# Optimization experiments

Measured on AMD Instinct MI355X. Metric: run time of the kernel, lower is better.

## Reference

```python
import jax, jax.numpy as jnp
import numpy as np
import math

NUM_HEADS = 16
ROPE_BASE = 10000.0
SLIDING_WINDOW = 512  # note: original triu-then-tril composition makes the mask empty (no-op)


def _rope_cos_sin(seq_len, head_dim, dtype):
    inv_freq = 1.0 / (ROPE_BASE ** (jnp.arange(0, head_dim, 2, dtype=jnp.float32) / head_dim))
    t = jnp.arange(seq_len, dtype=jnp.float32)
    freqs = t[:, None] * inv_freq[None, :]          # [S, D/2]
    emb = jnp.concatenate([freqs, freqs], axis=-1)  # [S, D]
    # reshape to broadcast over [B, S, H, D]
    return jnp.cos(emb)[None, :, None, :].astype(dtype), jnp.sin(emb)[None, :, None, :].astype(dtype)


def _rotate_half(x):
    x1, x2 = jnp.split(x, 2, axis=-1)
    return jnp.concatenate([-x2, x1], axis=-1)


def setup_inputs() -> dict:
    key = jax.random.key(0)
    ks = jax.random.split(key, 9)
    B, S, E = 2, 2048, 2048
    sc = 1.0 / math.sqrt(E)
    return {
        "hidden_states": jax.random.normal(ks[0], (B, S, E), dtype=jnp.float32),
        "Wq": jax.random.normal(ks[1], (E, E), dtype=jnp.float32) * sc,
        "bq": jax.random.normal(ks[2], (E,), dtype=jnp.float32) * 0.01,
        "Wk": jax.random.normal(ks[3], (E, E), dtype=jnp.float32) * sc,
        "bk": jax.random.normal(ks[4], (E,), dtype=jnp.float32) * 0.01,
        "Wv": jax.random.normal(ks[5], (E, E), dtype=jnp.float32) * sc,
        "bv": jax.random.normal(ks[6], (E,), dtype=jnp.float32) * 0.01,
        "Wo": jax.random.normal(ks[7], (E, E), dtype=jnp.float32) * sc,
        "bo": jax.random.normal(ks[8], (E,), dtype=jnp.float32) * 0.01,
    }


def reference(hidden_states, Wq, bq, Wk, bk, Wv, bv, Wo, bo):
    B, S, E = hidden_states.shape
    H = NUM_HEADS
    D = E // H
    q = (hidden_states @ Wq.T + bq).reshape(B, S, H, D)
    k = (hidden_states @ Wk.T + bk).reshape(B, S, H, D)
    v = (hidden_states @ Wv.T + bv).reshape(B, S, H, D)

    cos, sin = _rope_cos_sin(S, D, q.dtype)
    q = q * cos + _rotate_half(q) * sin
    k = k * cos + _rotate_half(k) * sin

    scale = 1.0 / math.sqrt(D)
    scores = jnp.einsum("bqhd,bkhd->bhqk", q, k) * scale  # [B,H,S,S]
    # Faithful to source: triu(ones, +w) followed by tril(..., -w) is empty -> mask is a no-op.
    attn = jax.nn.softmax(scores, axis=-1)
    out = jnp.einsum("bhqk,bkhd->bqhd", attn, v).reshape(B, S, E)
    return out @ Wo.T + bo
```

## Files before the change

kernel.cpp:

```cpp
#include <hip/hip_runtime.h>
#include <hip/hip_bf16.h>

#define B_ 2
#define S_ 2048
#define E_ 2048
#define H_ 16
#define D_ 128
#define M_ (B_*S_)
#define NQKV_ (3*E_)

typedef __attribute__((ext_vector_type(8))) short bf16x8;
typedef __attribute__((ext_vector_type(4))) float f32x4;
typedef __attribute__((ext_vector_type(4))) unsigned short u16x4;
typedef __attribute__((ext_vector_type(2))) unsigned u32x2;

__device__ __forceinline__ unsigned short f2bf(float f) {
  union { float f; unsigned u; } v; v.f = f;
  unsigned r = v.u + 0x7fffu + ((v.u >> 16) & 1u);
  return (unsigned short)(r >> 16);
}
__device__ __forceinline__ float bf2f(unsigned short h) {
  union { unsigned u; float f; } v; v.u = ((unsigned)h) << 16;
  return v.f;
}

__device__ __forceinline__ void gload_lds16(const void* g, void* l) {
  __builtin_amdgcn_global_load_lds(
      (const __attribute__((address_space(1))) unsigned*)g,
      (__attribute__((address_space(3))) unsigned*)l, 16, 0, 0);
}

__global__ __launch_bounds__(256) void prep_kernel(
    const float* __restrict__ hs,
    const float* __restrict__ Wq, const float* __restrict__ Wk, const float* __restrict__ Wv,
    const float* __restrict__ Wo,
    const float* __restrict__ bq, const float* __restrict__ bk, const float* __restrict__ bv,
    unsigned short* __restrict__ hsb, unsigned short* __restrict__ Wqkv,
    unsigned short* __restrict__ Wob, float* __restrict__ biasqkv,
    float* __restrict__ cosT, float* __restrict__ sinT)
{
  const int seg = blockIdx.y;
  const int t0 = blockIdx.x * 256 + threadIdx.x;
  const int stride = gridDim.x * 256;
  if (seg == 0) {
    const int n = (M_*E_)/4;
    for (int i = t0; i < n; i += stride) {
      f32x4 v = ((const f32x4*)hs)[i];
      u16x4 o; o[0]=f2bf(v[0]); o[1]=f2bf(v[1]); o[2]=f2bf(v[2]); o[3]=f2bf(v[3]);
      ((u16x4*)hsb)[i] = o;
    }
  } else if (seg == 1) {
    const int n = (3*E_*E_)/4;
    for (int i = t0; i < n; i += stride) {
      int e4 = i << 2;
      int r = e4 >> 11;
      int k = e4 & 2047;
      const float* src = (r < E_) ? (Wq + ((size_t)r << 11) + k)
                       : (r < 2*E_) ? (Wk + ((size_t)(r - E_) << 11) + k)
                       : (Wv + ((size_t)(r - 2*E_) << 11) + k);
      f32x4 v = *(const f32x4*)src;
      u16x4 o; o[0]=f2bf(v[0]); o[1]=f2bf(v[1]); o[2]=f2bf(v[2]); o[3]=f2bf(v[3]);
      ((u16x4*)Wqkv)[i] = o;
    }
  } else if (seg == 2) {
    const int n = (E_*E_)/4;
    for (int i = t0; i < n; i += stride) {
      f32x4 v = ((const f32x4*)Wo)[i];
      u16x4 o; o[0]=f2bf(v[0]); o[1]=f2bf(v[1]); o[2]=f2bf(v[2]); o[3]=f2bf(v[3]);
      ((u16x4*)Wob)[i] = o;
    }
  } else if (seg == 3) {
    for (int i = t0; i < NQKV_; i += stride)
      biasqkv[i] = (i < E_) ? bq[i] : (i < 2*E_) ? bk[i - E_] : bv[i - 2*E_];
  } else {
    for (int i = t0; i < S_*64; i += stride) {
      int j = i & 63, s = i >> 6;
      float inv = exp2f(-(float)j * (13.287712379549449f / 64.0f));
      float ang = (float)s * inv;
      cosT[i] = cosf(ang);
      sinT[i] = sinf(ang);
    }
  }
}

#define STAGE8(basePtr, BUF, AB, KS, KT) do { \
    unsigned short* dst_ = lds + (BUF)*32768 + (AB)*16384 + (KS)*8192; \
    const unsigned short* src_ = (basePtr) + (KT)*64 + (KS)*32; \
    _Pragma("unroll") \
    for (int j_ = 0; j_ < 2; ++j_) { \
      int cc_ = (j_ << 9) + tid; \
      int row_ = cc_ >> 2, c2_ = cc_ & 3; \
      int sc_ = c2_ ^ ((row_ >> 1) & 3); \
      gload_lds16(src_ + (size_t)row_*K + sc_*8, (char*)dst_ + cc_*16); \
    } } while(0)

#define LDA8(DST, MH, KS, BUF) do { \
    const unsigned short* Ab_ = lds + (BUF)*32768 + (KS)*8192; \
    _Pragma("unroll") \
    for (int j_ = 0; j_ < 4; ++j_) { \
      int row_ = wr*128 + ((MH)*4 + j_)*16 + l15; \
      DST[j_] = *(const bf16x8*)(Ab_ + row_*32 + ((l4 ^ ((row_>>1)&3)) << 3)); \
    } } while(0)

#define LDB8(DST, KS, BUF) do { \
    const unsigned short* Bb_ = lds + (BUF)*32768 + 16384 + (KS)*8192; \
    _Pragma("unroll") \
    for (int j_ = 0; j_ < 4; ++j_) { \
      int row_ = wc*64 + j_*16 + l15; \
      DST[j_] = *(const bf16x8*)(Bb_ + row_*32 + ((l4 ^ ((row_>>1)&3)) << 3)); \
    } } while(0)

#define EPSW(col, row) ((col) ^ ((((row) >> 2) & 3) << 3))

__global__ __launch_bounds__(512, 2) void gemm8(
    const unsigned short* __restrict__ A,
    const unsigned short* __restrict__ Bm,
    const float* __restrict__ bias,
    unsigned short* __restrict__ Cv,
    const float* __restrict__ cosT, const float* __restrict__ sinT,
    int M, int N, int K, int ldc, int nq)
{
  __shared__ __align__(16) unsigned short lds[65536];
  const int tid = threadIdx.x;
  const int lane = tid & 63;
  const int w = tid >> 6;
  const int wr = w >> 2, wc = w & 3;
  const int l15 = lane & 15, l4 = lane >> 4;

  const int ntile = N >> 8;
  int wg = blockIdx.x;
  const int cpx = gridDim.x >> 3;
  wg = (wg & 7) * cpx + (wg >> 3);
  const int tm = wg / ntile, tn = wg % ntile;

  const unsigned short* Abase = A + ((size_t)tm*256)*K;
  const unsigned short* Bbase = Bm + ((size_t)tn*256)*K;

  f32x4 acc[8][4] = {};

  const int NT = K >> 6;

  STAGE8(Bbase, 0, 1, 0, 0); STAGE8(Abase, 0, 0, 0, 0);
  STAGE8(Bbase, 0, 1, 1, 0); STAGE8(Abase, 0, 0, 1, 0);
  __builtin_amdgcn_sched_barrier(0);
  asm volatile("s_waitcnt vmcnt(0)" ::: "memory");
  __builtin_amdgcn_s_barrier();

  for (int t = 0; t < NT; ++t) {
    const int cb = t & 1;
    const bool more = (t + 1 < NT);
    if (more) {
      STAGE8(Bbase, cb^1, 1, 0, t+1); STAGE8(Abase, cb^1, 0, 0, t+1);
      STAGE8(Bbase, cb^1, 1, 1, t+1); STAGE8(Abase, cb^1, 0, 1, t+1);
    }
    __builtin_amdgcn_sched_barrier(0);
    #pragma unroll
    for (int ks = 0; ks < 2; ++ks) {
      bf16x8 a0[4], a1[4], bv[4];
      LDA8(a0, 0, ks, cb);
      LDA8(a1, 1, ks, cb);
      LDB8(bv, ks, cb);
      #pragma unroll
      for (int mm = 0; mm < 4; ++mm)
        #pragma unroll
        for (int nn = 0; nn < 4; ++nn)
          acc[mm][nn] = __builtin_amdgcn_mfma_f32_16x16x32_bf16(a0[mm], bv[nn], acc[mm][nn], 0,0,0);
      #pragma unroll
      for (int mm = 0; mm < 4; ++mm)
        #pragma unroll
        for (int nn = 0; nn < 4; ++nn)
          acc[4+mm][nn] = __builtin_amdgcn_mfma_f32_16x16x32_bf16(a1[mm], bv[nn], acc[4+mm][nn], 0,0,0);
    }
    if (more) {
      asm volatile("s_waitcnt vmcnt(0)" ::: "memory");
      __builtin_amdgcn_s_barrier();
    }
  }

  const bool isQ = (tn*256) < nq;
  const float QSC = 0.08838834764831845f * 1.4426950408889634f;

  __syncthreads();

  #pragma unroll
  for (int mt = 0; mt < 8; ++mt) {
    #pragma unroll
    for (int nt = 0; nt < 4; ++nt) {
      int col = wc*64 + nt*16 + l15;
      float bvv = bias[tn*256 + col];
      #pragma unroll
      for (int r = 0; r < 4; ++r) {
        int row = wr*128 + mt*16 + l4*4 + r;
        lds[row*256 + EPSW(col, row)] = f2bf(acc[mt][nt][r] + bvv);
      }
    }
  }
  __syncthreads();

  #pragma unroll
  for (int mt = 0; mt < 8; ++mt) {
    #pragma unroll
    for (int nt = 0; nt < 4; ++nt) {
      int col = wc*64 + nt*16 + l15;
      int colg = tn*256 + col;
      int j = col & 63;
      bool hi = (col >> 6) & 1;
      float bvv = bias[colg];
      #pragma unroll
      for (int r = 0; r < 4; ++r) {
        int row = wr*128 + mt*16 + l4*4 + r;
        int rowg = tm*256 + row;
        int s = rowg & (S_-1);
        float x = bf2f(f2bf(acc[mt][nt][r] + bvv));
        float pp = bf2f(lds[row*256 + EPSW(col ^ 64, row)]);
        float c = cosT[s*64 + j], sn = sinT[s*64 + j];
        float o = hi ? (x*c + pp*sn) : (x*c - pp*sn);
        if (isQ) o *= QSC;
        Cv[(size_t)rowg*ldc + colg] = f2bf(o);
      }
    }
  }
}

#define STGA(BUFP, TKT, KS) do { \
    unsigned short* dst_ = lds + (BUFP)*24576 + (KS)*4096; \
    const unsigned short* src_ = Abase + (TKT)*64 + (KS)*32; \
    int cc_ = tid; int row_ = cc_ >> 2, c2_ = cc_ & 3; \
    int sc_ = c2_ ^ ((row_ >> 1) & 3); \
    gload_lds16(src_ + (size_t)row_*K + sc_*8, (char*)dst_ + cc_*16); \
  } while(0)

#define STGB(BUFP, TKT, KS) do { \
    unsigned short* dst_ = lds + (BUFP)*24576 + 8192 + (KS)*8192; \
    const unsigned short* src_ = Bbase + (TKT)*64 + (KS)*32; \
    _Pragma("unroll") \
    for (int j_ = 0; j_ < 2; ++j_) { \
      int cc_ = (j_ << 9) + tid; int row_ = cc_ >> 2, c2_ = cc_ & 3; \
      int sc_ = c2_ ^ ((row_ >> 1) & 3); \
      gload_lds16(src_ + (size_t)row_*K + sc_*8, (char*)dst_ + cc_*16); \
    } } while(0)

template<int OUT_F32>
__global__ __launch_bounds__(512, 2) void gemmA(
    const unsigned short* __restrict__ A,
    const unsigned short* __restrict__ Bm,
    const float* __restrict__ bias,
    void* __restrict__ Cv,
    int M, int N, int K, int ldc)
{
  __shared__ __align__(16) unsigned short lds[73728];
  const int tid = threadIdx.x;
  const int lane = tid & 63;
  const int w = tid >> 6;
  const int wr = w >> 2, wc = w & 3;
  const int l15 = lane & 15, l4 = lane >> 4;

  const int ntile = N >> 8;
  int wg = blockIdx.x;
  const int cpx = gridDim.x >> 3;
  wg = (wg & 7) * cpx + (wg >> 3);
  const int tm = wg / ntile, tn = wg % ntile;

  const unsigned short* Abase = A + ((size_t)tm*128)*K;
  const unsigned short* Bbase = Bm + ((size_t)tn*256)*K;

  f32x4 acc[4][4] = {};

  const int NT = K >> 6;

  STGA(0,0,0); STGB(0,0,0); STGA(0,0,1); STGB(0,0,1);
  STGA(1,1,0); STGB(1,1,0); STGA(1,1,1); STGB(1,1,1);
  __builtin_amdgcn_sched_barrier(0);
  asm volatile("s_waitcnt vmcnt(6)" ::: "memory");
  __builtin_amdgcn_s_barrier();

  int bufc = 0, bufn = 2;
  for (int i = 0; i < NT; ++i) {
    const bool st = (i + 2 < NT);
    const bool more = (i + 1 < NT);
    if (st) { STGA(bufn, i+2, 0); STGB(bufn, i+2, 0); STGA(bufn, i+2, 1); STGB(bufn, i+2, 1); }
    __builtin_amdgcn_sched_barrier(0);
    #pragma unroll
    for (int ks = 0; ks < 2; ++ks) {
      bf16x8 af[4], bv[4];
      { const unsigned short* Ab_ = lds + bufc*24576 + ks*4096;
        #pragma unroll
        for (int j = 0; j < 4; ++j) {
          int row = wr*64 + j*16 + l15;
          af[j] = *(const bf16x8*)(Ab_ + row*32 + ((l4 ^ ((row>>1)&3)) << 3)); }
        const unsigned short* Bb_ = lds + bufc*24576 + 8192 + ks*8192;
        #pragma unroll
        for (int j = 0; j < 4; ++j) {
          int row = wc*64 + j*16 + l15;
          bv[j] = *(const bf16x8*)(Bb_ + row*32 + ((l4 ^ ((row>>1)&3)) << 3)); } }
      #pragma unroll
      for (int mm = 0; mm < 4; ++mm)
        #pragma unroll
        for (int nn = 0; nn < 4; ++nn)
          acc[mm][nn] = __builtin_amdgcn_mfma_f32_16x16x32_bf16(af[mm], bv[nn], acc[mm][nn], 0,0,0);
    }
    if (st)       { asm volatile("s_waitcnt vmcnt(6)" ::: "memory"); }
    else if (more){ asm volatile("s_waitcnt vmcnt(0)" ::: "memory"); }
    if (more) __builtin_amdgcn_s_barrier();
    bufc = (bufc + 1 == 3) ? 0 : bufc + 1;
    bufn = (bufn + 1 == 3) ? 0 : bufn + 1;
  }

  #pragma unroll
  for (int mt = 0; mt < 4; ++mt) {
    #pragma unroll
    for (int nt = 0; nt < 4; ++nt) {
      int colg = tn*256 + wc*64 + nt*16 + l15;
      float bvv = bias[colg];
      #pragma unroll
      for (int r = 0; r < 4; ++r) {
        int rowg = tm*128 + wr*64 + mt*16 + l4*4 + r;
        float v = acc[mt][nt][r] + bvv;
        if (OUT_F32) ((float*)Cv)[(size_t)rowg*ldc + colg] = v;
        else ((unsigned short*)Cv)[(size_t)rowg*ldc + colg] = f2bf(v);
      }
    }
  }
}

__global__ __launch_bounds__(256) void transv_kernel(
    const unsigned short* __restrict__ qkv, unsigned short* __restrict__ Vt)
{
  __shared__ unsigned short t[32][33];
  int bid = blockIdx.x;
  int st = bid & 63;
  int dt = (bid >> 6) & 3;
  int bh = bid >> 8;
  int b = bh >> 4, h = bh & 15;
  int tx = threadIdx.x & 31, ty = threadIdx.x >> 5;
  #pragma unroll
  for (int j = 0; j < 4; ++j) {
    int r = ty + j*8;
    t[r][tx] = qkv[(size_t)(b*S_ + st*32 + r)*NQKV_ + 2*E_ + h*128 + dt*32 + tx];
  }
  __syncthreads();
  #pragma unroll
  for (int j = 0; j < 4; ++j) {
    int r = ty + j*8;
    Vt[((size_t)bh*D_ + dt*32 + r)*S_ + st*32 + tx] = t[tx][r];
  }
}

__global__ __launch_bounds__(256, 2) void attn_kernel(
    const unsigned short* __restrict__ qkv, const unsigned short* __restrict__ Vt,
    unsigned short* __restrict__ Ao)
{
  __shared__ unsigned short lK[2][64*128];
  __shared__ unsigned short lV[2][128*64];
  __shared__ __align__(16) unsigned short lP[4*32*64];
  int bid = blockIdx.x;
  bid = (bid & 7)*64 + (bid >> 3);
  const int qt = bid & 15;
  const int bh = bid >> 4;
  const int b = bh >> 4, h = bh & 15;
  const int tid = threadIdx.x, lane = tid & 63, w = tid >> 6;
  const int l15 = lane & 15, l4 = lane >> 4;

  bf16x8 qf[2][4];
  #pragma unroll
  for (int g = 0; g < 2; ++g) {
    const int qrow = qt*128 + w*32 + g*16 + l15;
    const unsigned short* qp = qkv + (size_t)(b*S_ + qrow)*NQKV_ + h*128 + l4*8;
    #pragma unroll
    for (int f = 0; f < 4; ++f) qf[g][f] = *(const bf16x8*)(qp + f*32);
  }

  f32x4 O[2][8];
  #pragma unroll
  for (int g = 0; g < 2; ++g)
    #pragma unroll
    for (int i = 0; i < 8; ++i) O[g][i] = (f32x4){0.f,0.f,0.f,0.f};
  float mx[2] = {-1e30f,-1e30f}, lsum[2] = {0.f,0.f};

  unsigned short* myP = lP + w*(32*64);
  const int ksw = (l15 & 7) << 3;
  const size_t kbase = (size_t)b*S_*NQKV_ + E_ + (size_t)h*128;
  const size_t vbase = (size_t)bh*D_*S_;

  #define ASTAGE(bi, ktile) do { \
    _Pragma("unroll") \
    for (int i_ = 0; i_ < 4; ++i_) { \
      int cc_ = i_*256 + tid; \
      int row_ = cc_ >> 4, col_ = cc_ & 15; \
      int scol_ = col_ ^ (row_ & 7); \
      gload_lds16(qkv + kbase + (size_t)((ktile)*64 + row_)*NQKV_ + scol_*8, \
                  (char*)(&lK[bi][0]) + cc_*16); \
    } \
    _Pragma("unroll") \
    for (int i_ = 0; i_ < 4; ++i_) { \
      int cc_ = i_*256 + tid; \
      int row_ = cc_ >> 3, col_ = cc_ & 7; \
      int scol_ = col_ ^ ((row_ & 7) ^ ((row_ >> 3) & 7)); \
      gload_lds16(Vt + vbase + (size_t)row_*S_ + (ktile)*64 + scol_*8, \
                  (char*)(&lV[bi][0]) + cc_*16); \
    } } while(0)

  ASTAGE(0, 0);
  asm volatile("s_waitcnt vmcnt(0)" ::: "memory");
  __syncthreads();

  for (int it = 0; it < S_/64; ++it) {
    const int cur = it & 1;
    if (it + 1 < S_/64) ASTAGE(cur ^ 1, it + 1);
    __builtin_amdgcn_sched_barrier(0);

    f32x4 sfr[2][4];
    __builtin_amdgcn_s_setprio(1);
    #pragma unroll
    for (int nf = 0; nf < 4; ++nf) {
      f32x4 s0 = (f32x4){0.f,0.f,0.f,0.f};
      f32x4 s1 = (f32x4){0.f,0.f,0.f,0.f};
      #pragma unroll
      for (int ks = 0; ks < 4; ++ks) {
        int row = nf*16 + l15;
        int ch = (ks*4 + l4) ^ (row & 7);
        bf16x8 kf = *(const bf16x8*)(&lK[cur][0] + row*128 + ch*8);
        s0 = __builtin_amdgcn_mfma_f32_16x16x32_bf16(kf, qf[0][ks], s0, 0, 0, 0);
        s1 = __builtin_amdgcn_mfma_f32_16x16x32_bf16(kf, qf[1][ks], s1, 0, 0, 0);
      }
      sfr[0][nf] = s0; sfr[1][nf] = s1;
    }
    __builtin_amdgcn_s_setprio(0);

    float vm[2];
    #pragma unroll
    for (int g = 0; g < 2; ++g) {
      float v = -1e30f;
      #pragma unroll
      for (int nf = 0; nf < 4; ++nf)
        #pragma unroll
        for (int r = 0; r < 4; ++r) v = fmaxf(v, sfr[g][nf][r]);
      v = fmaxf(v, __shfl_xor(v, 16, 64));
      v = fmaxf(v, __shfl_xor(v, 32, 64));
      vm[g] = v;
    }

    if (__any((vm[0] > mx[0] + 8.0f) || (vm[1] > mx[1] + 8.0f))) {
      #pragma unroll
      for (int g = 0; g < 2; ++g) {
        float mn = fmaxf(mx[g], vm[g]);
        float al = __builtin_amdgcn_exp2f(mx[g] - mn);
        mx[g] = mn;
        lsum[g] *= al;
        #pragma unroll
        for (int r = 0; r < 4; ++r) {
          float ar = __shfl(al, (lane & 48) + l4*4 + r, 64);
          #pragma unroll
          for (int df = 0; df < 8; ++df) O[g][df][r] *= ar;
        }
      }
    }

    #pragma unroll
    for (int g = 0; g < 2; ++g) {
      float ps = 0.f;
      #pragma unroll
      for (int nf = 0; nf < 4; ++nf) {
        #pragma unroll
        for (int r = 0; r < 4; ++r) {
          float p = __builtin_amdgcn_exp2f(sfr[g][nf][r] - mx[g]);
          sfr[g][nf][r] = p;
          ps += p;
        }
      }
      ps += __shfl_xor(ps, 16, 64);
      ps += __shfl_xor(ps, 32, 64);
      lsum[g] += ps;
    }

    #pragma unroll
    for (int g = 0; g < 2; ++g) {
      #pragma unroll
      for (int nf = 0; nf < 4; ++nf) {
        unsigned lo, hi;
        asm("v_cvt_pk_bf16_f32 %0, %1, %2" : "=v"(lo) : "v"(sfr[g][nf][0]), "v"(sfr[g][nf][1]));
        asm("v_cvt_pk_bf16_f32 %0, %1, %2" : "=v"(hi) : "v"(sfr[g][nf][2]), "v"(sfr[g][nf][3]));
        int k0 = (nf*16 + l4*4) ^ ksw;
        u32x2 val; val[0] = lo; val[1] = hi;
        *(u32x2*)(myP + (g*16 + l15)*64 + k0) = val;
      }
    }
    asm volatile("s_waitcnt lgkmcnt(0)" ::: "memory");

    __builtin_amdgcn_s_setprio(1);
    #pragma unroll
    for (int ks2 = 0; ks2 < 2; ++ks2) {
      int kk = (ks2*32 + l4*8) ^ ksw;
      bf16x8 pf0 = *(const bf16x8*)(myP + l15*64 + kk);
      bf16x8 pf1 = *(const bf16x8*)(myP + (16 + l15)*64 + kk);
      #pragma unroll
      for (int df = 0; df < 8; ++df) {
        int row = df*16 + l15;
        int ch = (ks2*4 + l4) ^ ((row & 7) ^ ((row >> 3) & 7));
        bf16x8 vf = *(const bf16x8*)(&lV[cur][0] + row*64 + ch*8);
        O[0][df] = __builtin_amdgcn_mfma_f32_16x16x32_bf16(pf0, vf, O[0][df], 0, 0, 0);
        O[1][df] = __builtin_amdgcn_mfma_f32_16x16x32_bf16(pf1, vf, O[1][df], 0, 0, 0);
      }
    }
    __builtin_amdgcn_s_setprio(0);
    asm volatile("s_waitcnt vmcnt(0)" ::: "memory");
    __syncthreads();
  }

  #pragma unroll
  for (int g = 0; g < 2; ++g) {
    float linv = 1.0f / lsum[g];
    float inv[4];
    #pragma unroll
    for (int r = 0; r < 4; ++r) inv[r] = __shfl(linv, (lane & 48) + l4*4 + r, 64);
    #pragma unroll
    for (int df = 0; df < 8; ++df) {
      int colg = h*128 + df*16 + l15;
      #pragma unroll
      for (int r = 0; r < 4; ++r) {
        int rowg = qt*128 + w*32 + g*16 + l4*4 + r;
        Ao[(size_t)(b*S_ + rowg)*E_ + colg] = f2bf(O[g][df][r] * inv[r]);
      }
    }
  }
}

extern "C" void kernel_launch(void* const* d_in, const int* in_sizes, int n_in,
                              void* d_out, int out_size, void* d_ws, size_t ws_size,
                              hipStream_t stream) {
  const float* hs = (const float*)d_in[0];
  const float* Wq = (const float*)d_in[1];
  const float* bq = (const float*)d_in[2];
  const float* Wk = (const float*)d_in[3];
  const float* bk = (const float*)d_in[4];
  const float* Wv = (const float*)d_in[5];
  const float* bv = (const float*)d_in[6];
  const float* Wo = (const float*)d_in[7];
  const float* bo = (const float*)d_in[8];
  float* out = (float*)d_out;

  char* p = (char*)d_ws;
  auto alloc = [&](size_t bytes) { char* r = p; p += (bytes + 255) & ~(size_t)255; return r; };
  unsigned short* hsb  = (unsigned short*)alloc((size_t)M_*E_*2);
  unsigned short* Wqkv = (unsigned short*)alloc((size_t)NQKV_*E_*2);
  unsigned short* Wob  = (unsigned short*)alloc((size_t)E_*E_*2);
  unsigned short* qkv  = (unsigned short*)alloc((size_t)M_*NQKV_*2);
  unsigned short* Vt   = (unsigned short*)alloc((size_t)B_*H_*D_*S_*2);
  unsigned short* Ao   = (unsigned short*)alloc((size_t)M_*E_*2);
  float* biasqkv = (float*)alloc((size_t)NQKV_*4);
  float* cosT = (float*)alloc((size_t)S_*64*4);
  float* sinT = (float*)alloc((size_t)S_*64*4);

  prep_kernel<<<dim3(2048, 5), 256, 0, stream>>>(hs, Wq, Wk, Wv, Wo, bq, bk, bv,
      hsb, Wqkv, Wob, biasqkv, cosT, sinT);
  gemm8<<<dim3((M_/256)*(2*E_/256)), 512, 0, stream>>>(
      hsb, Wqkv, biasqkv, qkv, cosT, sinT, M_, 2*E_, E_, NQKV_, E_);
  gemmA<0><<<dim3((M_/128)*(E_/256)), 512, 0, stream>>>(
      hsb, Wqkv + (size_t)2*E_*E_, biasqkv + 2*E_, qkv + 2*E_, M_, E_, E_, NQKV_);
  transv_kernel<<<dim3(B_*H_*(D_/32)*(S_/32)), 256, 0, stream>>>(qkv, Vt);
  attn_kernel<<<dim3(B_*H_*(S_/128)), 256, 0, stream>>>(qkv, Vt, Ao);
  gemmA<1><<<dim3((M_/128)*(E_/256)), 512, 0, stream>>>(
      Ao, Wob, bo, out, M_, E_, E_, E_);
}
```

Baseline: 272.1 us.

## Fuse V transpose into V projection GEMM epilogue via LDS

Replaces the separate V GEMM plus transpose kernel with a single GEMM whose epilogue stages the bf16 tile in swizzled LDS and writes V directly in the transposed [B,H,D,S] layout. This removes one kernel launch and a full read and write of V through global memory. The K loop is moved into a shared macro so both GEMMs reuse it. The epilogue adds an extra LDS round trip and barrier, and the qkv V slice is no longer written.

After: 264.9 us. 1.03x faster.

```diff
diff --git a/kernel.cpp b/kernel.cpp
--- a/kernel.cpp
+++ b/kernel.cpp
@@ -240,6 +240,44 @@
       gload_lds16(src_ + (size_t)row_*K + sc_*8, (char*)dst_ + cc_*16); \
     } } while(0)
 
+#define GEMMA_KLOOP() do { \
+  STGA(0,0,0); STGB(0,0,0); STGA(0,0,1); STGB(0,0,1); \
+  STGA(1,1,0); STGB(1,1,0); STGA(1,1,1); STGB(1,1,1); \
+  __builtin_amdgcn_sched_barrier(0); \
+  asm volatile("s_waitcnt vmcnt(6)" ::: "memory"); \
+  __builtin_amdgcn_s_barrier(); \
+  int bufc = 0, bufn = 2; \
+  for (int i = 0; i < NT; ++i) { \
+    const bool st = (i + 2 < NT); \
+    const bool more = (i + 1 < NT); \
+    if (st) { STGA(bufn, i+2, 0); STGB(bufn, i+2, 0); STGA(bufn, i+2, 1); STGB(bufn, i+2, 1); } \
+    __builtin_amdgcn_sched_barrier(0); \
+    _Pragma("unroll") \
+    for (int ks = 0; ks < 2; ++ks) { \
+      bf16x8 af[4], bvv[4]; \
+      { const unsigned short* Ab_ = lds + bufc*24576 + ks*4096; \
+        _Pragma("unroll") \
+        for (int j = 0; j < 4; ++j) { \
+          int row = wr*64 + j*16 + l15; \
+          af[j] = *(const bf16x8*)(Ab_ + row*32 + ((l4 ^ ((row>>1)&3)) << 3)); } \
+        const unsigned short* Bb_ = lds + bufc*24576 + 8192 + ks*8192; \
+        _Pragma("unroll") \
+        for (int j = 0; j < 4; ++j) { \
+          int row = wc*64 + j*16 + l15; \
+          bvv[j] = *(const bf16x8*)(Bb_ + row*32 + ((l4 ^ ((row>>1)&3)) << 3)); } } \
+      _Pragma("unroll") \
+      for (int mm = 0; mm < 4; ++mm) \
+        _Pragma("unroll") \
+        for (int nn = 0; nn < 4; ++nn) \
+          acc[mm][nn] = __builtin_amdgcn_mfma_f32_16x16x32_bf16(af[mm], bvv[nn], acc[mm][nn], 0,0,0); \
+    } \
+    if (st)       { asm volatile("s_waitcnt vmcnt(6)" ::: "memory"); } \
+    else if (more){ asm volatile("s_waitcnt vmcnt(0)" ::: "memory"); } \
+    if (more) __builtin_amdgcn_s_barrier(); \
+    bufc = (bufc + 1 == 3) ? 0 : bufc + 1; \
+    bufn = (bufn + 1 == 3) ? 0 : bufn + 1; \
+  } } while(0)
+
 template<int OUT_F32>
 __global__ __launch_bounds__(512, 2) void gemmA(
     const unsigned short* __restrict__ A,
@@ -265,46 +303,9 @@
   const unsigned short* Bbase = Bm + ((size_t)tn*256)*K;
 
   f32x4 acc[4][4] = {};
-
   const int NT = K >> 6;
 
-  STGA(0,0,0); STGB(0,0,0); STGA(0,0,1); STGB(0,0,1);
-  STGA(1,1,0); STGB(1,1,0); STGA(1,1,1); STGB(1,1,1);
-  __builtin_amdgcn_sched_barrier(0);
-  asm volatile("s_waitcnt vmcnt(6)" ::: "memory");
-  __builtin_amdgcn_s_barrier();
-
-  int bufc = 0, bufn = 2;
-  for (int i = 0; i < NT; ++i) {
-    const bool st = (i + 2 < NT);
-    const bool more = (i + 1 < NT);
-    if (st) { STGA(bufn, i+2, 0); STGB(bufn, i+2, 0); STGA(bufn, i+2, 1); STGB(bufn, i+2, 1); }
-    __builtin_amdgcn_sched_barrier(0);
-    #pragma unroll
-    for (int ks = 0; ks < 2; ++ks) {
-      bf16x8 af[4], bv[4];
-      { const unsigned short* Ab_ = lds + bufc*24576 + ks*4096;
-        #pragma unroll
-        for (int j = 0; j < 4; ++j) {
-          int row = wr*64 + j*16 + l15;
-          af[j] = *(const bf16x8*)(Ab_ + row*32 + ((l4 ^ ((row>>1)&3)) << 3)); }
-        const unsigned short* Bb_ = lds + bufc*24576 + 8192 + ks*8192;
-        #pragma unroll
-        for (int j = 0; j < 4; ++j) {
-          int row = wc*64 + j*16 + l15;
-          bv[j] = *(const bf16x8*)(Bb_ + row*32 + ((l4 ^ ((row>>1)&3)) << 3)); } }
-      #pragma unroll
-      for (int mm = 0; mm < 4; ++mm)
-        #pragma unroll
-        for (int nn = 0; nn < 4; ++nn)
-          acc[mm][nn] = __builtin_amdgcn_mfma_f32_16x16x32_bf16(af[mm], bv[nn], acc[mm][nn], 0,0,0);
-    }
-    if (st)       { asm volatile("s_waitcnt vmcnt(6)" ::: "memory"); }
-    else if (more){ asm volatile("s_waitcnt vmcnt(0)" ::: "memory"); }
-    if (more) __builtin_amdgcn_s_barrier();
-    bufc = (bufc + 1 == 3) ? 0 : bufc + 1;
-    bufn = (bufn + 1 == 3) ? 0 : bufn + 1;
-  }
+  GEMMA_KLOOP();
 
   #pragma unroll
   for (int mt = 0; mt < 4; ++mt) {
@@ -323,26 +324,64 @@
   }
 }
 
-__global__ __launch_bounds__(256) void transv_kernel(
-    const unsigned short* __restrict__ qkv, unsigned short* __restrict__ Vt)
+__global__ __launch_bounds__(512, 2) void gemmVt(
+    const unsigned short* __restrict__ A,
+    const unsigned short* __restrict__ Bm,
+    const float* __restrict__ bias,
+    unsigned short* __restrict__ Vt,
+    int M, int N, int K)
 {
-  __shared__ unsigned short t[32][33];
-  int bid = blockIdx.x;
-  int st = bid & 63;
-  int dt = (bid >> 6) & 3;
-  int bh = bid >> 8;
-  int b = bh >> 4, h = bh & 15;
-  int tx = threadIdx.x & 31, ty = threadIdx.x >> 5;
-  #pragma unroll
-  for (int j = 0; j < 4; ++j) {
-    int r = ty + j*8;
-    t[r][tx] = qkv[(size_t)(b*S_ + st*32 + r)*NQKV_ + 2*E_ + h*128 + dt*32 + tx];
-  }
+  __shared__ __align__(16) unsigned short lds[73728];
+  const int tid = threadIdx.x;
+  const int lane = tid & 63;
+  const int w = tid >> 6;
+  const int wr = w >> 2, wc = w & 3;
+  const int l15 = lane & 15, l4 = lane >> 4;
+
+  const int ntile = N >> 8;
+  int wg = blockIdx.x;
+  const int cpx = gridDim.x >> 3;
+  wg = (wg & 7) * cpx + (wg >> 3);
+  const int tm = wg / ntile, tn = wg % ntile;
+
+  const unsigned short* Abase = A + ((size_t)tm*128)*K;
+  const unsigned short* Bbase = Bm + ((size_t)tn*256)*K;
+
+  f32x4 acc[4][4] = {};
+  const int NT = K >> 6;
+
+  GEMMA_KLOOP();
+
   __syncthreads();
   #pragma unroll
-  for (int j = 0; j < 4; ++j) {
-    int r = ty + j*8;
-    Vt[((size_t)bh*D_ + dt*32 + r)*S_ + st*32 + tx] = t[tx][r];
+  for (int mt = 0; mt < 4; ++mt) {
+    #pragma unroll
+    for (int nt = 0; nt < 4; ++nt) {
+      int col = wc*64 + nt*16 + l15;
+      float bvv = bias[tn*256 + col];
+      int row0 = wr*64 + mt*16 + l4*4;
+      u16x4 pk;
+      #pragma unroll
+      for (int r = 0; r < 4; ++r) pk[r] = f2bf(acc[mt][nt][r] + bvv);
+      *(u16x4*)(lds + col*128 + (row0 ^ ((col & 15) << 2))) = pk;
+    }
+  }
+  __syncthreads();
+
+  const int bb = (tm*128) >> 11;
+  const int s0 = (tm*128) & (S_-1);
+  #pragma unroll
+  for (int cc = 0; cc < 8; ++cc) {
+    int colL = w*32 + cc*4 + l4;
+    int colg = tn*256 + colL;
+    int h = colg >> 7, d = colg & 127;
+    int sw = (colL & 15) << 2;
+    int r0 = l15*8;
+    u16x4 lo = *(const u16x4*)(lds + colL*128 + (r0 ^ sw));
+    u16x4 hi = *(const u16x4*)(lds + colL*128 + ((r0 + 4) ^ sw));
+    unsigned short* dst = Vt + ((size_t)((bb*16 + h)*128 + d))*S_ + s0 + r0;
+    *(u16x4*)dst = lo;
+    *(u16x4*)(dst + 4) = hi;
   }
 }
 
@@ -555,9 +594,8 @@
       hsb, Wqkv, Wob, biasqkv, cosT, sinT);
   gemm8<<<dim3((M_/256)*(2*E_/256)), 512, 0, stream>>>(
       hsb, Wqkv, biasqkv, qkv, cosT, sinT, M_, 2*E_, E_, NQKV_, E_);
-  gemmA<0><<<dim3((M_/128)*(E_/256)), 512, 0, stream>>>(
-      hsb, Wqkv + (size_t)2*E_*E_, biasqkv + 2*E_, qkv + 2*E_, M_, E_, E_, NQKV_);
-  transv_kernel<<<dim3(B_*H_*(D_/32)*(S_/32)), 256, 0, stream>>>(qkv, Vt);
+  gemmVt<<<dim3((M_/128)*(E_/256)), 512, 0, stream>>>(
+      hsb, Wqkv + (size_t)2*E_*E_, biasqkv + 2*E_, Vt, M_, E_, E_);
   attn_kernel<<<dim3(B_*H_*(S_/128)), 256, 0, stream>>>(qkv, Vt, Ao);
   gemmA<1><<<dim3((M_/128)*(E_/256)), 512, 0, stream>>>(
       Ao, Wob, bo, out, M_, E_, E_, E_);
```
